# Kernel tuning notes

Measured on AMD Instinct MI355X. Metric: run time of the kernel, lower is better.

The kernel has to match this reference:

```python
import jax, jax.numpy as jnp
import numpy as np

# Static problem configuration
NUM_GRAPHS = 64
NODES_PER_GRAPH = 2048          # divisible by OUT_H
NODE_EMB_DIM = 256              # divisible by OUT_W
COND_EMB_DIM = 64
OUT_H, OUT_W = 16, 8            # AdaptiveAvgPool2d output -> pooled dim H*W = 128
MLP_H = 256
BN_EPS = 1e-5


def setup_inputs() -> dict:
    key = jax.random.key(0)
    ks = jax.random.split(key, 8)
    N = NUM_GRAPHS * NODES_PER_GRAPH
    x = jax.random.normal(ks[0], (N, NODE_EMB_DIM), dtype=jnp.float32)
    # equal contiguous segments: node i belongs to graph i // NODES_PER_GRAPH
    batch = jnp.repeat(jnp.arange(NUM_GRAPHS, dtype=jnp.int64), NODES_PER_GRAPH)
    conditioner_z_ref = jax.random.normal(ks[1], (N, COND_EMB_DIM), dtype=jnp.float32)
    mlp_in = COND_EMB_DIM + OUT_H * OUT_W
    W1 = jax.random.normal(ks[2], (mlp_in, MLP_H), dtype=jnp.float32) / np.sqrt(mlp_in)
    b1 = jnp.zeros((MLP_H,), dtype=jnp.float32)
    gamma = jnp.ones((MLP_H,), dtype=jnp.float32)
    beta = jnp.zeros((MLP_H,), dtype=jnp.float32)
    W2 = jax.random.normal(ks[3], (MLP_H, 3), dtype=jnp.float32) / np.sqrt(MLP_H)
    b2 = jnp.zeros((3,), dtype=jnp.float32)
    return {"x": x, "batch": batch, "conditioner_z_ref": conditioner_z_ref,
            "W1": W1, "b1": b1, "gamma": gamma, "beta": beta, "W2": W2, "b2": b2}


def _adaptive_pool(x):
    # x: [N_total, D] with equal contiguous segments of NODES_PER_GRAPH rows per graph.
    # AdaptiveAvgPool2d((OUT_H, OUT_W)) on each [n, D] "image"; since n % OUT_H == 0
    # and D % OUT_W == 0 the adaptive bins are uniform -> exact reshape-mean.
    B = x.shape[0] // NODES_PER_GRAPH
    xg = x.reshape(B, OUT_H, NODES_PER_GRAPH // OUT_H, OUT_W, NODE_EMB_DIM // OUT_W)
    pooled = xg.mean(axis=(2, 4))                 # [B, OUT_H, OUT_W]
    return pooled.reshape(B, OUT_H * OUT_W)       # [B, H*W]


def reference(x, batch, conditioner_z_ref, W1, b1, gamma, beta, W2, b2):
    batch_pooled = _adaptive_pool(x)                          # [B, H*W]
    gathered = batch_pooled[batch]                            # [N, H*W]
    h = jnp.concatenate([conditioner_z_ref, gathered], axis=1)  # [N, cond + H*W]
    # Linear -> BatchNorm1d (training-mode batch stats, biased var) -> GELU (exact)
    h = h @ W1 + b1                                           # [N, MLP_H]
    mean = h.mean(axis=0)
    var = h.var(axis=0)
    h = (h - mean) * jax.lax.rsqrt(var + BN_EPS) * gamma + beta
    h = jax.nn.gelu(h, approximate=False)
    return h @ W2 + b2                                        # [N, 3]
```

## Files before the change

### kernel.cpp

```cpp
#include <hip/hip_runtime.h>
#include <math.h>

#define NG    64
#define NPG   2048
#define NTOT  (NG*NPG)
#define ZD    64
#define PD    128
#define MH    256

typedef __attribute__((ext_vector_type(8))) short bf16x8;
typedef __attribute__((ext_vector_type(4))) float f32x4;

__device__ __forceinline__ unsigned short f2bf(float f){
  unsigned u = __float_as_uint(f);
  unsigned r = u + 0x7FFFu + ((u >> 16) & 1u);
  return (unsigned short)(r >> 16);
}
__device__ __forceinline__ float bf2f(unsigned short s){
  return __uint_as_float(((unsigned)s) << 16);
}
__device__ __forceinline__ float gelu_f(float x){
  float t = 0.7978845608028654f * fmaf(0.044715f * x, x * x, x);
  float e = __expf(2.0f * t);
  float th = 1.0f - 2.0f / (e + 1.0f);
  return 0.5f * x * (1.0f + th);
}

__launch_bounds__(256)
__global__ void k1_pool_zstat(const float* __restrict__ x, const float* __restrict__ z,
                              float* __restrict__ pooled, float* __restrict__ St,
                              float* __restrict__ C){
  __shared__ __align__(16) unsigned short s_zt[64 * 264];
  __shared__ float s_cred[4096];
  int tid = threadIdx.x;

  if (blockIdx.x >= 256){
    int bi = blockIdx.x - 256;
    int b  = bi >> 4;
    int oh = bi & 15;
    int c4 = tid & 63;
    int rq = tid >> 6;
    const float4* x4 = (const float4*)x;
    size_t base = (size_t)(b * NPG + oh * 128) * 64;
    float4 acc = make_float4(0.f, 0.f, 0.f, 0.f);
    #pragma unroll 8
    for (int i = 0; i < 32; i++){
      float4 v = x4[base + (size_t)(rq + i * 4) * 64 + c4];
      acc.x += v.x; acc.y += v.y; acc.z += v.z; acc.w += v.w;
    }
    s_cred[tid] = acc.x + acc.y + acc.z + acc.w;
    __syncthreads();
    if (tid < 8){
      float s = 0.f;
      #pragma unroll
      for (int w = 0; w < 4; w++)
        #pragma unroll
        for (int j = 0; j < 8; j++)
          s += s_cred[w * 64 + tid * 8 + j];
      pooled[b * PD + oh * 8 + tid] = s * (1.0f / 4096.0f);
    }
    return;
  }

  int blk = blockIdx.x;
  int g = blk >> 2, q4 = blk & 3;
  int lane = tid & 63, wave = tid >> 6;
  int col = lane & 15, quad = lane >> 4;
  const float4* z4 = (const float4*)z + ((size_t)g * 2048 + q4 * 512) * 16;
  int d4 = tid & 15;

  f32x4 acc[4][4];
  #pragma unroll
  for (int a = 0; a < 4; a++)
    #pragma unroll
    for (int b = 0; b < 4; b++) acc[a][b] = (f32x4)(0.f);
  float s0 = 0.f, s1 = 0.f, s2 = 0.f, s3 = 0.f;

  for (int ch = 0; ch < 2; ch++){
    #pragma unroll
    for (int i = 0; i < 16; i++){
      int idx = tid + i * 256;
      int m = idx >> 4;
      float4 v = z4[ch * 4096 + idx];
      s0 += v.x; s1 += v.y; s2 += v.z; s3 += v.w;
      s_zt[(d4 * 4 + 0) * 264 + m] = f2bf(v.x);
      s_zt[(d4 * 4 + 1) * 264 + m] = f2bf(v.y);
      s_zt[(d4 * 4 + 2) * 264 + m] = f2bf(v.z);
      s_zt[(d4 * 4 + 3) * 264 + m] = f2bf(v.w);
    }
    __syncthreads();
    #pragma unroll
    for (int ks = 0; ks < 2; ks++){
      int k0 = wave * 64 + ks * 32;
      bf16x8 fr[4];
      #pragma unroll
      for (int t = 0; t < 4; t++)
        fr[t] = *(const bf16x8*)&s_zt[(t * 16 + col) * 264 + k0 + quad * 8];
      #pragma unroll
      for (int mt = 0; mt < 4; mt++)
        #pragma unroll
        for (int nt = 0; nt < 4; nt++)
          acc[mt][nt] = __builtin_amdgcn_mfma_f32_16x16x32_bf16(fr[mt], fr[nt], acc[mt][nt], 0, 0, 0);
    }
    __syncthreads();
  }

  s0 += __shfl_xor(s0, 16); s0 += __shfl_xor(s0, 32);
  s1 += __shfl_xor(s1, 16); s1 += __shfl_xor(s1, 32);
  s2 += __shfl_xor(s2, 16); s2 += __shfl_xor(s2, 32);
  s3 += __shfl_xor(s3, 16); s3 += __shfl_xor(s3, 32);
  if (quad == 0){
    atomicAdd(&St[(d4 * 4 + 0) * 64 + g], s0);
    atomicAdd(&St[(d4 * 4 + 1) * 64 + g], s1);
    atomicAdd(&St[(d4 * 4 + 2) * 64 + g], s2);
    atomicAdd(&St[(d4 * 4 + 3) * 64 + g], s3);
  }

  #pragma unroll
  for (int w = 0; w < 4; w++){
    if (wave == w){
      #pragma unroll
      for (int mt = 0; mt < 4; mt++)
        #pragma unroll
        for (int nt = 0; nt < 4; nt++)
          #pragma unroll
          for (int r = 0; r < 4; r++){
            int p = mt * 16 + quad * 4 + r;
            int qc = nt * 16 + col;
            if (w == 0) s_cred[p * 64 + qc]  = acc[mt][nt][r];
            else        s_cred[p * 64 + qc] += acc[mt][nt][r];
          }
    }
    __syncthreads();
  }
  for (int f = tid; f < 4096; f += 256)
    atomicAdd(&C[f], s_cred[f]);
}

__launch_bounds__(256)
__global__ void k2_stats(const float* __restrict__ pooled, const float* __restrict__ W1,
                         const float* __restrict__ b1, const float* __restrict__ gamma,
                         const float* __restrict__ beta, const float* __restrict__ C,
                         const float* __restrict__ St, float* __restrict__ Aj,
                         float* __restrict__ cprime, unsigned short* __restrict__ Wbf){
  __shared__ float pl[64 * 129];
  int tid = threadIdx.x;
  int jc = tid >> 6, lane = tid & 63;
  int j = blockIdx.x * 4 + jc;

  Wbf[(size_t)j * 64 + lane] = f2bf(W1[(size_t)lane * 256 + j]);

  for (int idx = tid; idx < 8192; idx += 256)
    pl[(idx >> 7) * 129 + (idx & 127)] = pooled[idx];
  __syncthreads();

  float g = b1[j];
  #pragma unroll 8
  for (int k = 0; k < 128; k++)
    g = fmaf(pl[lane * 129 + k], W1[(size_t)(ZD + k) * MH + j], g);

  float wl = W1[(size_t)lane * MH + j];
  float t1 = 0.f, t2 = 0.f;
  #pragma unroll
  for (int q = 0; q < 64; q++){
    float wq = __uint_as_float(__builtin_amdgcn_readlane(__float_as_uint(wl), q));
    t1 = fmaf(C [q * 64 + lane], wq, t1);
    t2 = fmaf(St[q * 64 + lane], wq, t2);
  }
  float v_wcw = wl * t1;
  float v_gs  = g * t2;
  float v_s   = t2;
  float v_g   = g;
  float v_g2  = g * g;
  #pragma unroll
  for (int off = 32; off; off >>= 1){
    v_wcw += __shfl_xor(v_wcw, off);
    v_gs  += __shfl_xor(v_gs , off);
    v_s   += __shfl_xor(v_s  , off);
    v_g   += __shfl_xor(v_g  , off);
    v_g2  += __shfl_xor(v_g2 , off);
  }
  const float invN = 1.0f / (float)NTOT;
  float mean = v_s * invN + v_g * (1.0f / 64.0f);
  float eh2  = v_wcw * invN + 2.0f * invN * v_gs + v_g2 * (1.0f / 64.0f);
  float var  = eh2 - mean * mean;
  float aj = gamma[j] * rsqrtf(var + 1e-5f);
  if (lane == 0) Aj[j] = aj;
  cprime[lane * MH + j] = fmaf(aj, g, beta[j] - aj * mean);
}

__launch_bounds__(256, 2)
__global__ void final_kernel(const float* __restrict__ z, const unsigned short* __restrict__ Wbf,
                             const float* __restrict__ Aj, const float* __restrict__ cp,
                             const float* __restrict__ W2, const float* __restrict__ b2,
                             float* __restrict__ out){
  __shared__ __align__(16) unsigned short zt[128 * 136];
  __shared__ float slab[2][384];
  int tid = threadIdx.x;
  int n0 = blockIdx.x * 128;
  int g = blockIdx.x >> 4;

  const float4* z4 = (const float4*)z + (size_t)n0 * 16;
  #pragma unroll
  for (int i = 0; i < 8; i++){
    int idx = tid + i * 256;
    int m = idx >> 4, d4 = idx & 15;
    float4 v = z4[idx];
    ushort4 h, l;
    h.x = f2bf(v.x); l.x = f2bf(v.x - bf2f(h.x));
    h.y = f2bf(v.y); l.y = f2bf(v.y - bf2f(h.y));
    h.z = f2bf(v.z); l.z = f2bf(v.z - bf2f(h.z));
    h.w = f2bf(v.w); l.w = f2bf(v.w - bf2f(h.w));
    *(ushort4*)&zt[m * 136 + d4 * 4]      = h;
    *(ushort4*)&zt[m * 136 + 64 + d4 * 4] = l;
  }
  __syncthreads();

  int lane = tid & 63, wave = tid >> 6;
  int wm = wave & 1, wn = wave >> 1;
  int col = lane & 15, quad = lane >> 4;
  int mbase = wm * 64, nbase = wn * 128;

  f32x4 acc[4][8];
  #pragma unroll
  for (int mt = 0; mt < 4; mt++)
    #pragma unroll
    for (int nt = 0; nt < 8; nt++) acc[mt][nt] = (f32x4)(0.f);

  #pragma unroll
  for (int ks = 0; ks < 4; ks++){
    int k0 = ks * 32;
    bf16x8 af[4];
    #pragma unroll
    for (int mt = 0; mt < 4; mt++)
      af[mt] = *(const bf16x8*)&zt[(mbase + mt * 16 + col) * 136 + k0 + quad * 8];
    #pragma unroll
    for (int nt = 0; nt < 8; nt++){
      bf16x8 bv = *(const bf16x8*)&Wbf[(size_t)(nbase + nt * 16 + col) * 64 + (ks & 1) * 32 + quad * 8];
      #pragma unroll
      for (int mt = 0; mt < 4; mt++)
        acc[mt][nt] = __builtin_amdgcn_mfma_f32_16x16x32_bf16(af[mt], bv, acc[mt][nt], 0, 0, 0);
    }
  }

  float aj[8], cj[8], w2a[8], w2b[8], w2c[8];
  #pragma unroll
  for (int nt = 0; nt < 8; nt++){
    int j = nbase + nt * 16 + col;
    aj[nt] = Aj[j];
    cj[nt] = cp[g * MH + j];
    w2a[nt] = W2[j * 3 + 0];
    w2b[nt] = W2[j * 3 + 1];
    w2c[nt] = W2[j * 3 + 2];
  }

  #pragma unroll
  for (int mt = 0; mt < 4; mt++){
    #pragma unroll
    for (int r = 0; r < 4; r++){
      float o0 = 0.f, o1 = 0.f, o2 = 0.f;
      #pragma unroll
      for (int nt = 0; nt < 8; nt++){
        float h  = fmaf(aj[nt], acc[mt][nt][r], cj[nt]);
        float ge = gelu_f(h);
        o0 = fmaf(ge, w2a[nt], o0);
        o1 = fmaf(ge, w2b[nt], o1);
        o2 = fmaf(ge, w2c[nt], o2);
      }
      #pragma unroll
      for (int off = 8; off; off >>= 1){
        o0 += __shfl_xor(o0, off);
        o1 += __shfl_xor(o1, off);
        o2 += __shfl_xor(o2, off);
      }
      if (col == 0){
        int node = mbase + mt * 16 + quad * 4 + r;
        slab[wn][node * 3 + 0] = o0;
        slab[wn][node * 3 + 1] = o1;
        slab[wn][node * 3 + 2] = o2;
      }
    }
  }
  __syncthreads();
  float b2v[3] = {b2[0], b2[1], b2[2]};
  for (int f = tid; f < 384; f += 256)
    out[(size_t)blockIdx.x * 384 + f] = slab[0][f] + slab[1][f] + b2v[f % 3];
}

extern "C" void kernel_launch(void* const* d_in, const int* in_sizes, int n_in,
                              void* d_out, int out_size, void* d_ws, size_t ws_size,
                              hipStream_t stream){
  (void)in_sizes; (void)n_in; (void)out_size; (void)ws_size;
  const float* x     = (const float*)d_in[0];
  const float* z     = (const float*)d_in[2];
  const float* W1    = (const float*)d_in[3];
  const float* b1    = (const float*)d_in[4];
  const float* gamma = (const float*)d_in[5];
  const float* beta  = (const float*)d_in[6];
  const float* W2    = (const float*)d_in[7];
  const float* b2    = (const float*)d_in[8];
  float* out = (float*)d_out;

  float* W = (float*)d_ws;
  float* pooled = W;
  float* St     = W + 8192;
  float* C      = W + 12288;
  float* Aj     = W + 16384;
  float* CP     = W + 16640;
  unsigned short* Wbf = (unsigned short*)(W + 33024);

  hipMemsetAsync((char*)d_ws + 8192 * 4, 0, 8192 * 4, stream);

  k1_pool_zstat<<<dim3(1280), dim3(256), 0, stream>>>(x, z, pooled, St, C);
  k2_stats     <<<dim3(64),   dim3(256), 0, stream>>>(pooled, W1, b1, gamma, beta, C, St, Aj, CP, Wbf);
  final_kernel <<<dim3(NTOT / 128), dim3(256), 0, stream>>>(z, Wbf, Aj, CP, W2, b2, out);
}
```

Baseline: 284.0 us.

## Swizzle z transpose in LDS and replace Gram atomics with partial-sum reduction

The z tile is now loaded as four rows per thread and stored to LDS as packed ushort4 words with an XOR swizzle, and the MFMA fragment reads use the matching swizzle. This is meant to cut the scalar LDS stores and bank conflicts of the old transpose. Each block's 64x64 Gram partial is written to a per-block workspace slice instead of being atomically added into C. A new 16-block kernel then sums those 256 slices, trading atomic contention for roughly 4 MB of extra workspace traffic and one more launch.

Measured after the change: 294.8 us. 3.8% more time.

```diff
diff --git a/kernel.cpp b/kernel.cpp
--- a/kernel.cpp
+++ b/kernel.cpp
@@ -29,7 +29,7 @@
 __launch_bounds__(256)
 __global__ void k1_pool_zstat(const float* __restrict__ x, const float* __restrict__ z,
                               float* __restrict__ pooled, float* __restrict__ St,
-                              float* __restrict__ C){
+                              float* __restrict__ Cpart){
   __shared__ __align__(16) unsigned short s_zt[64 * 264];
   __shared__ float s_cred[4096];
   int tid = threadIdx.x;
@@ -67,7 +67,8 @@
   int lane = tid & 63, wave = tid >> 6;
   int col = lane & 15, quad = lane >> 4;
   const float4* z4 = (const float4*)z + ((size_t)g * 2048 + q4 * 512) * 16;
-  int d4 = tid & 15;
+  int d4 = col;
+  int mg = quad;
 
   f32x4 acc[4][4];
   #pragma unroll
@@ -78,24 +79,51 @@
 
   for (int ch = 0; ch < 2; ch++){
     #pragma unroll
-    for (int i = 0; i < 16; i++){
-      int idx = tid + i * 256;
-      int m = idx >> 4;
-      float4 v = z4[ch * 4096 + idx];
-      s0 += v.x; s1 += v.y; s2 += v.z; s3 += v.w;
-      s_zt[(d4 * 4 + 0) * 264 + m] = f2bf(v.x);
-      s_zt[(d4 * 4 + 1) * 264 + m] = f2bf(v.y);
-      s_zt[(d4 * 4 + 2) * 264 + m] = f2bf(v.z);
-      s_zt[(d4 * 4 + 3) * 264 + m] = f2bf(v.w);
+    for (int rd = 0; rd < 4; rd++){
+      int m0 = rd * 64 + wave * 16 + mg * 4;
+      const float4* src = z4 + ch * 4096 + m0 * 16 + d4;
+      float4 v0 = src[0];
+      float4 v1 = src[16];
+      float4 v2 = src[32];
+      float4 v3 = src[48];
+      s0 += v0.x + v1.x + v2.x + v3.x;
+      s1 += v0.y + v1.y + v2.y + v3.y;
+      s2 += v0.z + v1.z + v2.z + v3.z;
+      s3 += v0.w + v1.w + v2.w + v3.w;
+      int slot = m0 >> 3;
+      int sub  = m0 & 4;
+      int d0 = d4 * 4;
+      {
+        int d = d0 + 0; int ss = slot ^ ((d >> 3) & 7);
+        ushort4 w = make_ushort4(f2bf(v0.x), f2bf(v1.x), f2bf(v2.x), f2bf(v3.x));
+        *(ushort4*)&s_zt[d * 264 + ss * 8 + sub] = w;
+      }
+      {
+        int d = d0 + 1; int ss = slot ^ ((d >> 3) & 7);
+        ushort4 w = make_ushort4(f2bf(v0.y), f2bf(v1.y), f2bf(v2.y), f2bf(v3.y));
+        *(ushort4*)&s_zt[d * 264 + ss * 8 + sub] = w;
+      }
+      {
+        int d = d0 + 2; int ss = slot ^ ((d >> 3) & 7);
+        ushort4 w = make_ushort4(f2bf(v0.z), f2bf(v1.z), f2bf(v2.z), f2bf(v3.z));
+        *(ushort4*)&s_zt[d * 264 + ss * 8 + sub] = w;
+      }
+      {
+        int d = d0 + 3; int ss = slot ^ ((d >> 3) & 7);
+        ushort4 w = make_ushort4(f2bf(v0.w), f2bf(v1.w), f2bf(v2.w), f2bf(v3.w));
+        *(ushort4*)&s_zt[d * 264 + ss * 8 + sub] = w;
+      }
     }
     __syncthreads();
     #pragma unroll
     for (int ks = 0; ks < 2; ks++){
-      int k0 = wave * 64 + ks * 32;
       bf16x8 fr[4];
       #pragma unroll
-      for (int t = 0; t < 4; t++)
-        fr[t] = *(const bf16x8*)&s_zt[(t * 16 + col) * 264 + k0 + quad * 8];
+      for (int t = 0; t < 4; t++){
+        int row = t * 16 + col;
+        int ss  = (wave * 8 + ks * 4 + quad) ^ ((row >> 3) & 7);
+        fr[t] = *(const bf16x8*)&s_zt[row * 264 + ss * 8];
+      }
       #pragma unroll
       for (int mt = 0; mt < 4; mt++)
         #pragma unroll
@@ -133,8 +161,19 @@
     }
     __syncthreads();
   }
+  float* Cp = Cpart + (size_t)blk * 4096;
   for (int f = tid; f < 4096; f += 256)
-    atomicAdd(&C[f], s_cred[f]);
+    Cp[f] = s_cred[f];
+}
+
+__launch_bounds__(256)
+__global__ void k1b_reduce(const float* __restrict__ Cpart, float* __restrict__ C){
+  int f = blockIdx.x * 256 + threadIdx.x;
+  float s = 0.f;
+  #pragma unroll 8
+  for (int b = 0; b < 256; b++)
+    s += Cpart[(size_t)b * 4096 + f];
+  C[f] = s;
 }
 
 __launch_bounds__(256)
@@ -308,10 +347,12 @@
   float* Aj     = W + 16384;
   float* CP     = W + 16640;
   unsigned short* Wbf = (unsigned short*)(W + 33024);
-
-  hipMemsetAsync((char*)d_ws + 8192 * 4, 0, 8192 * 4, stream);
-
-  k1_pool_zstat<<<dim3(1280), dim3(256), 0, stream>>>(x, z, pooled, St, C);
+  float* Cpart  = W + 41216;
+
+  hipMemsetAsync((char*)d_ws + 8192 * 4, 0, 4096 * 4, stream);
+
+  k1_pool_zstat<<<dim3(1280), dim3(256), 0, stream>>>(x, z, pooled, St, Cpart);
+  k1b_reduce   <<<dim3(16),   dim3(256), 0, stream>>>(Cpart, C);
   k2_stats     <<<dim3(64),   dim3(256), 0, stream>>>(pooled, W1, b1, gamma, beta, C, St, Aj, CP, Wbf);
   final_kernel <<<dim3(NTOT / 128), dim3(256), 0, stream>>>(z, Wbf, Aj, CP, W2, b2, out);
 }
```
